# Kernel tuning notes

Measured on AMD Instinct MI355X. Metric: run time of the kernel, lower is better.

The kernel has to match this reference:

```python
import jax, jax.numpy as jnp
import numpy as np

EMBED = 768
HEADS = 12


def setup_inputs() -> dict:
    key = jax.random.key(0)
    k1, k2, k3 = jax.random.split(key, 3)
    B, N, E = 2, 2048, EMBED
    x = jax.random.normal(k1, (B, N, E), dtype=jnp.float32)
    w_qkv = jax.random.normal(k2, (3 * E, E), dtype=jnp.float32) * (1.0 / np.sqrt(E))
    b_qkv = jnp.zeros((3 * E,), dtype=jnp.float32)
    w_o = jax.random.normal(k3, (E, E), dtype=jnp.float32) * (1.0 / np.sqrt(E))
    b_o = jnp.zeros((E,), dtype=jnp.float32)
    return {"x": x, "w_qkv": w_qkv, "b_qkv": b_qkv, "w_o": w_o, "b_o": b_o}


def reference(x, w_qkv, b_qkv, w_o, b_o):
    B, N, E = x.shape
    H = HEADS
    d = E // H
    # fused qkv projection (torch Linear: x @ W^T + b)
    qkv = x @ w_qkv.T + b_qkv                       # [B, N, 3E]
    # Rearrange 'b n (h qkv e) -> b qkv h n e'
    qkv = qkv.reshape(B, N, H, 3, d).transpose(0, 3, 2, 1, 4)  # [B, 3, H, N, d]
    q, k, v = qkv[:, 0], qkv[:, 1], qkv[:, 2]       # each [B, H, N, d]
    scores = jnp.einsum("bhqd,bhkd->bhqk", q, k)    # [B, H, N, N]
    attn = jax.nn.softmax(scores / jnp.sqrt(jnp.float32(E)), axis=-1)
    ctx = jnp.einsum("bhqk,bhkd->bhqd", attn, v)    # [B, H, N, d]
    ctx = ctx.transpose(0, 2, 1, 3).reshape(B, N, E)  # 'b h n d -> b n (h d)'
    out = ctx @ w_o.T + b_o
    return out
```

## Files before the change

### kernel.cpp

```cpp
#include <hip/hip_runtime.h>

#define BB 2
#define NN 2048
#define EE 768
#define HH 12
#define DD 64
#define MM (BB*NN)
#define E3 (3*EE)
#define QSCALE 0.05205877280961602f

typedef __bf16 bf16x8 __attribute__((ext_vector_type(8)));
typedef float  f32x4  __attribute__((ext_vector_type(4)));
typedef unsigned short u16x8 __attribute__((ext_vector_type(8)));

#define MFMA(a,b,c) __builtin_amdgcn_mfma_f32_16x16x32_bf16(a,b,c,0,0,0)

__device__ __forceinline__ unsigned short f2bf(float f) {
    unsigned int u = __float_as_uint(f);
    u += 0x7FFFu + ((u >> 16) & 1u);
    return (unsigned short)(u >> 16);
}

typedef __attribute__((address_space(3))) unsigned int as3u32;
typedef __attribute__((address_space(1))) unsigned int as1u32;
__device__ __forceinline__ void gll16(const void* g, void* l) {
    __builtin_amdgcn_global_load_lds((const as1u32*)(uintptr_t)g,
                                     (as3u32*)(unsigned int)(uintptr_t)l, 16, 0, 0);
}

__global__ __launch_bounds__(256)
void cast_bf16(const float* __restrict__ s, unsigned short* __restrict__ d, int n4) {
    int i = blockIdx.x * 256 + threadIdx.x;
    if (i < n4) {
        float4 v = ((const float4*)s)[i];
        ushort4 o;
        o.x = f2bf(v.x); o.y = f2bf(v.y); o.z = f2bf(v.z); o.w = f2bf(v.w);
        ((ushort4*)d)[i] = o;
    }
}

template<int MODE>
__global__ __launch_bounds__(256)
void gemm_bf16(const unsigned short* __restrict__ A, const unsigned short* __restrict__ W,
               const float* __restrict__ bias,
               unsigned short* __restrict__ o0, unsigned short* __restrict__ o1,
               unsigned short* __restrict__ o2, float* __restrict__ of, int Kd)
{
    __shared__ unsigned short As[128 * 32];
    __shared__ unsigned short Bs[128 * 32];

    const int tid = threadIdx.x;
    const int l = tid & 63;
    const int w = tid >> 6;
    const int m0 = blockIdx.x * 128;
    const int c0 = blockIdx.y * 128;
    const int wm = (w >> 1) * 64;
    const int wn = (w & 1) * 64;

    const int s0 = w * 2;
    const unsigned short* a_src0 = A + (size_t)(m0 + s0*16      + (l>>2)) * Kd + (l&3)*8;
    const unsigned short* a_src1 = A + (size_t)(m0 + (s0+1)*16  + (l>>2)) * Kd + (l&3)*8;
    const unsigned short* b_src0 = W + (size_t)(c0 + s0*16      + (l>>2)) * Kd + (l&3)*8;
    const unsigned short* b_src1 = W + (size_t)(c0 + (s0+1)*16  + (l>>2)) * Kd + (l&3)*8;
    unsigned short* a_dst0 = &As[s0*512];
    unsigned short* a_dst1 = &As[(s0+1)*512];
    unsigned short* b_dst0 = &Bs[s0*512];
    unsigned short* b_dst1 = &Bs[(s0+1)*512];

    const f32x4 zero4 = {0.f, 0.f, 0.f, 0.f};
    f32x4 acc[4][4];
    #pragma unroll
    for (int i = 0; i < 4; ++i)
        #pragma unroll
        for (int j = 0; j < 4; ++j) acc[i][j] = zero4;

    for (int k0 = 0; k0 < Kd; k0 += 32) {
        __syncthreads();
        gll16(a_src0 + k0, a_dst0);
        gll16(a_src1 + k0, a_dst1);
        gll16(b_src0 + k0, b_dst0);
        gll16(b_src1 + k0, b_dst1);
        __syncthreads();

        bf16x8 af[4], bf[4];
        #pragma unroll
        for (int i = 0; i < 4; ++i)
            af[i] = *(const bf16x8*)&As[(wm + 16*i + (l&15))*32 + (l>>4)*8];
        #pragma unroll
        for (int j = 0; j < 4; ++j)
            bf[j] = *(const bf16x8*)&Bs[(wn + 16*j + (l&15))*32 + (l>>4)*8];
        #pragma unroll
        for (int i = 0; i < 4; ++i)
            #pragma unroll
            for (int j = 0; j < 4; ++j)
                acc[i][j] = MFMA(af[i], bf[j], acc[i][j]);
    }

    if (MODE == 0) {
        #pragma unroll
        for (int j = 0; j < 4; ++j) {
            const int col = c0 + wn + 16*j + (l&15);
            const float bj = bias[col];
            #pragma unroll
            for (int i = 0; i < 4; ++i) {
                #pragma unroll
                for (int r = 0; r < 4; ++r) {
                    const int row = m0 + wm + 16*i + (l>>4)*4 + r;
                    of[(size_t)row * EE + col] = acc[i][j][r] + bj;
                }
            }
        }
    } else {
        const int sec = (c0 + wn) >> 6;
        const int hh = sec / 3;
        const int tt = sec - hh*3;
        #pragma unroll
        for (int j = 0; j < 4; ++j) {
            const int col = c0 + wn + 16*j + (l&15);
            const int dcol = 16*j + (l&15);
            const float bj = bias[col];
            #pragma unroll
            for (int i = 0; i < 4; ++i) {
                const int row0 = m0 + wm + 16*i + (l>>4)*4;
                const int b = row0 >> 11;
                const int n = row0 & (NN - 1);
                if (tt == 2) {
                    ushort4 pk;
                    pk.x = f2bf(acc[i][j][0] + bj);
                    pk.y = f2bf(acc[i][j][1] + bj);
                    pk.z = f2bf(acc[i][j][2] + bj);
                    pk.w = f2bf(acc[i][j][3] + bj);
                    *(ushort4*)&o2[(((size_t)b*HH + hh)*DD + dcol)*NN + n] = pk;
                } else {
                    unsigned short* dst = (tt == 0) ? o0 : o1;
                    #pragma unroll
                    for (int r = 0; r < 4; ++r) {
                        float val = acc[i][j][r] + bj;
                        if (tt == 0) val *= QSCALE;
                        dst[(((size_t)b*HH + hh)*NN + n + r)*DD + dcol] = f2bf(val);
                    }
                }
            }
        }
    }
}

__global__ __launch_bounds__(256)
void attn_mfma(const unsigned short* __restrict__ Q, const unsigned short* __restrict__ K,
               const unsigned short* __restrict__ Vt_g, unsigned short* __restrict__ ctx)
{
    __shared__ unsigned short Ks[64 * 72];
    __shared__ unsigned short Vt[64 * 72];
    __shared__ unsigned short Pq[4 * 16 * 72];

    const int tid = threadIdx.x;
    const int l = tid & 63;
    const int w = tid >> 6;
    const int quad = l >> 4;
    const int lc = l & 15;
    const int bq = blockIdx.x, h = blockIdx.y, b = blockIdx.z;
    const size_t hb = ((size_t)(b*HH + h)) * NN * DD;

    const f32x4 zero4 = {0.f, 0.f, 0.f, 0.f};

    const int qrow = bq*64 + w*16 + lc;
    const bf16x8 qf0 = *(const bf16x8*)(Q + hb + (size_t)qrow*DD +      quad*8);
    const bf16x8 qf1 = *(const bf16x8*)(Q + hb + (size_t)qrow*DD + 32 + quad*8);

    f32x4 o[4];
    #pragma unroll
    for (int dj = 0; dj < 4; ++dj) o[dj] = zero4;
    float lsum = 0.f;

    const int srow = tid >> 2;
    const int sc = tid & 3;
    const unsigned short* kbase = K + hb + (size_t)srow*DD + sc*16;
    const unsigned short* vbase = Vt_g + ((size_t)(b*HH + h)*DD + srow)*NN + sc*16;
    unsigned short* ksl = &Ks[srow*72 + sc*16];
    unsigned short* vsl = &Vt[srow*72 + sc*16];

    for (int kt = 0; kt < NN/64; ++kt) {
        const unsigned short* ksrc = kbase + (size_t)kt*64*DD;
        const unsigned short* vsrc = vbase + kt*64;
        u16x8 k0 = *(const u16x8*)ksrc;
        u16x8 k1 = *(const u16x8*)(ksrc + 8);
        u16x8 v0 = *(const u16x8*)vsrc;
        u16x8 v1 = *(const u16x8*)(vsrc + 8);
        __syncthreads();
        *(u16x8*)ksl = k0;
        *(u16x8*)(ksl + 8) = k1;
        *(u16x8*)vsl = v0;
        *(u16x8*)(vsl + 8) = v1;
        __syncthreads();

        f32x4 st[4];
        #pragma unroll
        for (int jf = 0; jf < 4; ++jf) {
            bf16x8 kf0 = *(const bf16x8*)&Ks[(16*jf + lc)*72 +      quad*8];
            bf16x8 kf1 = *(const bf16x8*)&Ks[(16*jf + lc)*72 + 32 + quad*8];
            f32x4 acc0 = MFMA(kf0, qf0, zero4);
            st[jf] = MFMA(kf1, qf1, acc0);
        }

        #pragma unroll
        for (int jf = 0; jf < 4; ++jf) {
            float e0 = __builtin_amdgcn_exp2f(st[jf][0]);
            float e1 = __builtin_amdgcn_exp2f(st[jf][1]);
            float e2 = __builtin_amdgcn_exp2f(st[jf][2]);
            float e3 = __builtin_amdgcn_exp2f(st[jf][3]);
            lsum += (e0 + e1) + (e2 + e3);
            ushort4 pk;
            pk.x = f2bf(e0); pk.y = f2bf(e1); pk.z = f2bf(e2); pk.w = f2bf(e3);
            *(ushort4*)&Pq[w*1152 + lc*72 + 16*jf + quad*4] = pk;
        }

        #pragma unroll
        for (int kb = 0; kb < 2; ++kb) {
            bf16x8 pf = *(const bf16x8*)&Pq[w*1152 + lc*72 + kb*32 + quad*8];
            #pragma unroll
            for (int dj = 0; dj < 4; ++dj) {
                bf16x8 vf = *(const bf16x8*)&Vt[(16*dj + lc)*72 + kb*32 + quad*8];
                o[dj] = MFMA(vf, pf, o[dj]);
            }
        }
    }

    lsum += __shfl_xor(lsum, 16);
    lsum += __shfl_xor(lsum, 32);
    const float inv = 1.f / lsum;

    const int n = bq*64 + w*16 + lc;
    #pragma unroll
    for (int dj = 0; dj < 4; ++dj) {
        ushort4 pk;
        pk.x = f2bf(o[dj][0] * inv);
        pk.y = f2bf(o[dj][1] * inv);
        pk.z = f2bf(o[dj][2] * inv);
        pk.w = f2bf(o[dj][3] * inv);
        *(ushort4*)&ctx[((size_t)(b*NN + n))*EE + h*DD + 16*dj + quad*4] = pk;
    }
}

extern "C" void kernel_launch(void* const* d_in, const int* in_sizes, int n_in,
                              void* d_out, int out_size, void* d_ws, size_t ws_size,
                              hipStream_t stream)
{
    const float* x     = (const float*)d_in[0];
    const float* w_qkv = (const float*)d_in[1];
    const float* b_qkv = (const float*)d_in[2];
    const float* w_o   = (const float*)d_in[3];
    const float* b_o   = (const float*)d_in[4];
    float* out = (float*)d_out;

    unsigned short* wsu = (unsigned short*)d_ws;
    const size_t XB = (size_t)MM * EE;
    const size_t WQ = (size_t)E3 * EE;
    const size_t WO = (size_t)EE * EE;
    const size_t HS = (size_t)BB * HH * NN * DD;
    unsigned short* xb   = wsu;
    unsigned short* wqb  = xb  + XB;
    unsigned short* wob  = wqb + WQ;
    unsigned short* qb   = wob + WO;
    unsigned short* kb   = qb  + HS;
    unsigned short* vtb  = kb  + HS;
    unsigned short* ctxb = vtb + HS;

    cast_bf16<<<(int)((XB/4 + 255)/256), 256, 0, stream>>>(x, xb, (int)(XB/4));
    cast_bf16<<<(int)((WQ/4 + 255)/256), 256, 0, stream>>>(w_qkv, wqb, (int)(WQ/4));
    cast_bf16<<<(int)((WO/4 + 255)/256), 256, 0, stream>>>(w_o, wob, (int)(WO/4));

    dim3 g1(MM/128, E3/128);
    gemm_bf16<1><<<g1, 256, 0, stream>>>(xb, wqb, b_qkv, qb, kb, vtb, nullptr, EE);

    dim3 g2(NN/64, HH, BB);
    attn_mfma<<<g2, 256, 0, stream>>>(qb, kb, vtb, ctxb);

    dim3 g3(MM/128, EE/128);
    gemm_bf16<0><<<g3, 256, 0, stream>>>(ctxb, wob, b_o, nullptr, nullptr, nullptr, out, EE);
}
```

Measured before the change: 180.3 us.

## Merge cast kernels, enlarge QKV GEMM tile, linearize attention grid

Folds the three fp32-to-bf16 cast launches into one kernel that picks its source by index. This relies on the workspace buffers for x, w_qkv and w_o being contiguous, which they are. The QKV projection gets its own kernel with a 256x128 tile, so each wave computes 128x64 and each weight tile loaded into LDS is reused across more rows. This costs twice the accumulator registers and yields fewer blocks. The attention grid becomes 1D with the batch-head index varying fastest, so concurrently running blocks of different heads interleave, and the output GEMM is specialized without the mode template.

```diff
diff --git a/kernel.cpp b/kernel.cpp
--- a/kernel.cpp
+++ b/kernel.cpp
@@ -28,23 +28,121 @@
                                      (as3u32*)(unsigned int)(uintptr_t)l, 16, 0, 0);
 }
 
+#define XB4 786432
+#define WQ4 442368
+#define WO4 147456
 __global__ __launch_bounds__(256)
-void cast_bf16(const float* __restrict__ s, unsigned short* __restrict__ d, int n4) {
+void cast3(const float* __restrict__ x, const float* __restrict__ wq,
+           const float* __restrict__ wo, unsigned short* __restrict__ dst) {
     int i = blockIdx.x * 256 + threadIdx.x;
-    if (i < n4) {
-        float4 v = ((const float4*)s)[i];
-        ushort4 o;
-        o.x = f2bf(v.x); o.y = f2bf(v.y); o.z = f2bf(v.z); o.w = f2bf(v.w);
-        ((ushort4*)d)[i] = o;
-    }
-}
-
-template<int MODE>
+    const float* src;
+    int off;
+    if (i < XB4)            { src = x;  off = i; }
+    else if (i < XB4+WQ4)   { src = wq; off = i - XB4; }
+    else                    { src = wo; off = i - XB4 - WQ4; }
+    float4 v = ((const float4*)src)[off];
+    ushort4 o;
+    o.x = f2bf(v.x); o.y = f2bf(v.y); o.z = f2bf(v.z); o.w = f2bf(v.w);
+    ((ushort4*)dst)[i] = o;
+}
+
 __global__ __launch_bounds__(256)
-void gemm_bf16(const unsigned short* __restrict__ A, const unsigned short* __restrict__ W,
-               const float* __restrict__ bias,
-               unsigned short* __restrict__ o0, unsigned short* __restrict__ o1,
-               unsigned short* __restrict__ o2, float* __restrict__ of, int Kd)
+void gemm_qkv(const unsigned short* __restrict__ A, const unsigned short* __restrict__ W,
+              const float* __restrict__ bias,
+              unsigned short* __restrict__ o0, unsigned short* __restrict__ o1,
+              unsigned short* __restrict__ o2)
+{
+    __shared__ unsigned short As[256 * 32];
+    __shared__ unsigned short Bs[128 * 32];
+
+    const int tid = threadIdx.x;
+    const int l = tid & 63;
+    const int w = tid >> 6;
+    const int m0 = blockIdx.x * 256;
+    const int c0 = blockIdx.y * 128;
+    const int wm = (w >> 1) * 128;
+    const int wn = (w & 1) * 64;
+
+    const unsigned short* a_src[4];
+    const unsigned short* b_src[2];
+    unsigned short* a_dst[4];
+    unsigned short* b_dst[2];
+    #pragma unroll
+    for (int s = 0; s < 4; ++s) {
+        a_src[s] = A + (size_t)(m0 + w*64 + s*16 + (l>>2)) * EE + (l&3)*8;
+        a_dst[s] = &As[(w*64 + s*16) * 32];
+    }
+    #pragma unroll
+    for (int s = 0; s < 2; ++s) {
+        b_src[s] = W + (size_t)(c0 + w*32 + s*16 + (l>>2)) * EE + (l&3)*8;
+        b_dst[s] = &Bs[(w*32 + s*16) * 32];
+    }
+
+    const f32x4 zero4 = {0.f, 0.f, 0.f, 0.f};
+    f32x4 acc[8][4];
+    #pragma unroll
+    for (int i = 0; i < 8; ++i)
+        #pragma unroll
+        for (int j = 0; j < 4; ++j) acc[i][j] = zero4;
+
+    for (int k0 = 0; k0 < EE; k0 += 32) {
+        __syncthreads();
+        #pragma unroll
+        for (int s = 0; s < 4; ++s) gll16(a_src[s] + k0, a_dst[s]);
+        #pragma unroll
+        for (int s = 0; s < 2; ++s) gll16(b_src[s] + k0, b_dst[s]);
+        __syncthreads();
+
+        bf16x8 af[8], bf[4];
+        #pragma unroll
+        for (int i = 0; i < 8; ++i)
+            af[i] = *(const bf16x8*)&As[(wm + 16*i + (l&15))*32 + (l>>4)*8];
+        #pragma unroll
+        for (int j = 0; j < 4; ++j)
+            bf[j] = *(const bf16x8*)&Bs[(wn + 16*j + (l&15))*32 + (l>>4)*8];
+        #pragma unroll
+        for (int i = 0; i < 8; ++i)
+            #pragma unroll
+            for (int j = 0; j < 4; ++j)
+                acc[i][j] = MFMA(af[i], bf[j], acc[i][j]);
+    }
+
+    const int sec = (c0 + wn) >> 6;
+    const int hh = sec / 3;
+    const int tt = sec - hh*3;
+    #pragma unroll
+    for (int j = 0; j < 4; ++j) {
+        const int col = c0 + wn + 16*j + (l&15);
+        const int dcol = 16*j + (l&15);
+        const float bj = bias[col];
+        #pragma unroll
+        for (int i = 0; i < 8; ++i) {
+            const int row0 = m0 + wm + 16*i + (l>>4)*4;
+            const int b = row0 >> 11;
+            const int n = row0 & (NN - 1);
+            if (tt == 2) {
+                ushort4 pk;
+                pk.x = f2bf(acc[i][j][0] + bj);
+                pk.y = f2bf(acc[i][j][1] + bj);
+                pk.z = f2bf(acc[i][j][2] + bj);
+                pk.w = f2bf(acc[i][j][3] + bj);
+                *(ushort4*)&o2[(((size_t)b*HH + hh)*DD + dcol)*NN + n] = pk;
+            } else {
+                unsigned short* dst = (tt == 0) ? o0 : o1;
+                #pragma unroll
+                for (int r = 0; r < 4; ++r) {
+                    float val = acc[i][j][r] + bj;
+                    if (tt == 0) val *= QSCALE;
+                    dst[(((size_t)b*HH + hh)*NN + n + r)*DD + dcol] = f2bf(val);
+                }
+            }
+        }
+    }
+}
+
+__global__ __launch_bounds__(256)
+void gemm_out(const unsigned short* __restrict__ A, const unsigned short* __restrict__ W,
+              const float* __restrict__ bias, float* __restrict__ of)
 {
     __shared__ unsigned short As[128 * 32];
     __shared__ unsigned short Bs[128 * 32];
@@ -58,10 +156,10 @@
     const int wn = (w & 1) * 64;
 
     const int s0 = w * 2;
-    const unsigned short* a_src0 = A + (size_t)(m0 + s0*16      + (l>>2)) * Kd + (l&3)*8;
-    const unsigned short* a_src1 = A + (size_t)(m0 + (s0+1)*16  + (l>>2)) * Kd + (l&3)*8;
-    const unsigned short* b_src0 = W + (size_t)(c0 + s0*16      + (l>>2)) * Kd + (l&3)*8;
-    const unsigned short* b_src1 = W + (size_t)(c0 + (s0+1)*16  + (l>>2)) * Kd + (l&3)*8;
+    const unsigned short* a_src0 = A + (size_t)(m0 + s0*16      + (l>>2)) * EE + (l&3)*8;
+    const unsigned short* a_src1 = A + (size_t)(m0 + (s0+1)*16  + (l>>2)) * EE + (l&3)*8;
+    const unsigned short* b_src0 = W + (size_t)(c0 + s0*16      + (l>>2)) * EE + (l&3)*8;
+    const unsigned short* b_src1 = W + (size_t)(c0 + (s0+1)*16  + (l>>2)) * EE + (l&3)*8;
     unsigned short* a_dst0 = &As[s0*512];
     unsigned short* a_dst1 = &As[(s0+1)*512];
     unsigned short* b_dst0 = &Bs[s0*512];
@@ -74,7 +172,7 @@
         #pragma unroll
         for (int j = 0; j < 4; ++j) acc[i][j] = zero4;
 
-    for (int k0 = 0; k0 < Kd; k0 += 32) {
+    for (int k0 = 0; k0 < EE; k0 += 32) {
         __syncthreads();
         gll16(a_src0 + k0, a_dst0);
         gll16(a_src1 + k0, a_dst1);
@@ -96,50 +194,16 @@
                 acc[i][j] = MFMA(af[i], bf[j], acc[i][j]);
     }
 
-    if (MODE == 0) {
-        #pragma unroll
-        for (int j = 0; j < 4; ++j) {
-            const int col = c0 + wn + 16*j + (l&15);
-            const float bj = bias[col];
+    #pragma unroll
+    for (int j = 0; j < 4; ++j) {
+        const int col = c0 + wn + 16*j + (l&15);
+        const float bj = bias[col];
+        #pragma unroll
+        for (int i = 0; i < 4; ++i) {
             #pragma unroll
-            for (int i = 0; i < 4; ++i) {
-                #pragma unroll
-                for (int r = 0; r < 4; ++r) {
-                    const int row = m0 + wm + 16*i + (l>>4)*4 + r;
-                    of[(size_t)row * EE + col] = acc[i][j][r] + bj;
-                }
-            }
-        }
-    } else {
-        const int sec = (c0 + wn) >> 6;
-        const int hh = sec / 3;
-        const int tt = sec - hh*3;
-        #pragma unroll
-        for (int j = 0; j < 4; ++j) {
-            const int col = c0 + wn + 16*j + (l&15);
-            const int dcol = 16*j + (l&15);
-            const float bj = bias[col];
-            #pragma unroll
-            for (int i = 0; i < 4; ++i) {
-                const int row0 = m0 + wm + 16*i + (l>>4)*4;
-                const int b = row0 >> 11;
-                const int n = row0 & (NN - 1);
-                if (tt == 2) {
-                    ushort4 pk;
-                    pk.x = f2bf(acc[i][j][0] + bj);
-                    pk.y = f2bf(acc[i][j][1] + bj);
-                    pk.z = f2bf(acc[i][j][2] + bj);
-                    pk.w = f2bf(acc[i][j][3] + bj);
-                    *(ushort4*)&o2[(((size_t)b*HH + hh)*DD + dcol)*NN + n] = pk;
-                } else {
-                    unsigned short* dst = (tt == 0) ? o0 : o1;
-                    #pragma unroll
-                    for (int r = 0; r < 4; ++r) {
-                        float val = acc[i][j][r] + bj;
-                        if (tt == 0) val *= QSCALE;
-                        dst[(((size_t)b*HH + hh)*NN + n + r)*DD + dcol] = f2bf(val);
-                    }
-                }
+            for (int r = 0; r < 4; ++r) {
+                const int row = m0 + wm + 16*i + (l>>4)*4 + r;
+                of[(size_t)row * EE + col] = acc[i][j][r] + bj;
             }
         }
     }
@@ -158,8 +222,13 @@
     const int w = tid >> 6;
     const int quad = l >> 4;
     const int lc = l & 15;
-    const int bq = blockIdx.x, h = blockIdx.y, b = blockIdx.z;
-    const size_t hb = ((size_t)(b*HH + h)) * NN * DD;
+
+    const int id = blockIdx.x;
+    const int bh = id % 24;
+    const int bq = id / 24;
+    const int b  = bh / 12;
+    const int h  = bh - b*12;
+    const size_t hb = (size_t)bh * NN * DD;
 
     const f32x4 zero4 = {0.f, 0.f, 0.f, 0.f};
 
@@ -175,7 +244,7 @@
     const int srow = tid >> 2;
     const int sc = tid & 3;
     const unsigned short* kbase = K + hb + (size_t)srow*DD + sc*16;
-    const unsigned short* vbase = Vt_g + ((size_t)(b*HH + h)*DD + srow)*NN + sc*16;
+    const unsigned short* vbase = Vt_g + ((size_t)bh*DD + srow)*NN + sc*16;
     unsigned short* ksl = &Ks[srow*72 + sc*16];
     unsigned short* vsl = &Vt[srow*72 + sc*16];
 
@@ -265,16 +334,13 @@
     unsigned short* vtb  = kb  + HS;
     unsigned short* ctxb = vtb + HS;
 
-    cast_bf16<<<(int)((XB/4 + 255)/256), 256, 0, stream>>>(x, xb, (int)(XB/4));
-    cast_bf16<<<(int)((WQ/4 + 255)/256), 256, 0, stream>>>(w_qkv, wqb, (int)(WQ/4));
-    cast_bf16<<<(int)((WO/4 + 255)/256), 256, 0, stream>>>(w_o, wob, (int)(WO/4));
-
-    dim3 g1(MM/128, E3/128);
-    gemm_bf16<1><<<g1, 256, 0, stream>>>(xb, wqb, b_qkv, qb, kb, vtb, nullptr, EE);
-
-    dim3 g2(NN/64, HH, BB);
-    attn_mfma<<<g2, 256, 0, stream>>>(qb, kb, vtb, ctxb);
+    cast3<<<(XB4 + WQ4 + WO4)/256, 256, 0, stream>>>(x, w_qkv, w_o, xb);
+
+    dim3 g1(MM/256, E3/128);
+    gemm_qkv<<<g1, 256, 0, stream>>>(xb, wqb, b_qkv, qb, kb, vtb);
+
+    attn_mfma<<<768, 256, 0, stream>>>(qb, kb, vtb, ctxb);
 
     dim3 g3(MM/128, EE/128);
-    gemm_bf16<0><<<g3, 256, 0, stream>>>(ctxb, wob, b_o, nullptr, nullptr, nullptr, out, EE);
-}
+    gemm_out<<<g3, 256, 0, stream>>>(ctxb, wob, b_o, out);
+}
```

Result: slower. 204.5 us (+13.4%).
